# Kernel tuning notes

Hardware: AMD Instinct MI355X
Metric: run time of the kernel (lower is better)

Reference implementation:

```python
import jax, jax.numpy as jnp
import numpy as np


def setup_inputs() -> dict:
    key = jax.random.key(0)
    ks = jax.random.split(key, 5)
    B, S, H, F, E = 2, 2048, 768, 1536, 8
    scale_h = 1.0 / np.sqrt(H)
    scale_f = 1.0 / np.sqrt(F)
    return {
        "hidden_states": jax.random.normal(ks[0], (B, S, H), dtype=jnp.float32),
        "gate_w": jax.random.normal(ks[1], (E, H), dtype=jnp.float32) * scale_h,
        "w1": jax.random.normal(ks[2], (E, F, H), dtype=jnp.float32) * scale_h,
        "w3": jax.random.normal(ks[3], (E, F, H), dtype=jnp.float32) * scale_h,
        "w2": jax.random.normal(ks[4], (E, H, F), dtype=jnp.float32) * scale_f,
        "k": 2,
    }


def reference(hidden_states, gate_w, w1, w3, w2, k):
    B, S, H = hidden_states.shape
    E = gate_w.shape[0]
    x = hidden_states.reshape(-1, H)                     # [T, H]
    T = x.shape[0]

    # Router: softmax in fp32, top-k, renormalize among selected experts.
    router_logits = x @ gate_w.T                         # [T, E]
    probs = jax.nn.softmax(router_logits.astype(jnp.float32), axis=-1)
    top_w, top_i = jax.lax.top_k(probs, k)               # [T, k]
    top_w = top_w / jnp.sum(top_w, axis=-1, keepdims=True)
    top_w = top_w.astype(x.dtype)

    # Scatter top-k weights into dense [T, E] combine weights (0 for unselected).
    combine = jnp.zeros((T, E), dtype=x.dtype)
    combine = combine.at[jnp.arange(T)[:, None], top_i].set(top_w)

    # SwiGLU experts (zero-weight experts contribute exactly 0 to the sum).
    g = jnp.einsum("th,efh->tef", x, w1)                 # [T, E, F]
    u = jnp.einsum("th,efh->tef", x, w3)                 # [T, E, F]
    act = jax.nn.silu(g) * u                             # [T, E, F]
    expert_out = jnp.einsum("tef,ehf->teh", act, w2)     # [T, E, H]
    y = jnp.einsum("te,teh->th", combine, expert_out)    # [T, H]

    return y.reshape(B, S, H), router_logits
```

## Files before the change

### kernel.cpp

```cpp
#include <hip/hip_runtime.h>
#include <hip/hip_bf16.h>

#define T_TOK 4096
#define H_DIM 768
#define E_NUM 8
#define F_DIM 1536
#define WELEM (E_NUM * F_DIM * H_DIM)

typedef __bf16 bf16x8 __attribute__((ext_vector_type(8)));
typedef float f32x4 __attribute__((ext_vector_type(4)));
typedef unsigned int u32;

#define VMCNT(n) asm volatile("s_waitcnt vmcnt(" #n ")" ::: "memory")
#define CFENCE() asm volatile("" ::: "memory")

__device__ __forceinline__ unsigned short f2bf(float f) {
    unsigned int u = __float_as_uint(f);
    u += 0x7FFF + ((u >> 16) & 1);
    return (unsigned short)(u >> 16);
}

__device__ __forceinline__ void gload16(const unsigned short* g, unsigned short* l) {
    __builtin_amdgcn_global_load_lds(
        (const __attribute__((address_space(1))) u32*)(g),
        (__attribute__((address_space(3))) u32*)(l),
        16, 0, 0);
}

__global__ void convert3_kernel(const float* __restrict__ s0,
                                const float* __restrict__ s1,
                                const float* __restrict__ s2,
                                unsigned short* __restrict__ d0,
                                unsigned short* __restrict__ d1,
                                unsigned short* __restrict__ d2) {
    int i = (blockIdx.x * blockDim.x + threadIdx.x) * 4;
    int stride = gridDim.x * blockDim.x * 4;
    for (; i < 3 * WELEM; i += stride) {
        int r = i / WELEM;
        int j = i - r * WELEM;
        const float* s = (r == 0) ? s0 : (r == 1) ? s1 : s2;
        unsigned short* d = (r == 0) ? d0 : (r == 1) ? d1 : d2;
        float4 v = *reinterpret_cast<const float4*>(s + j);
        ushort4 o;
        o.x = f2bf(v.x); o.y = f2bf(v.y); o.z = f2bf(v.z); o.w = f2bf(v.w);
        *reinterpret_cast<ushort4*>(d + j) = o;
    }
}

__global__ __launch_bounds__(256) void router_kernel(
    const float* __restrict__ x,
    const float* __restrict__ gw,
    float* __restrict__ logits_out,
    float* __restrict__ weight,
    int* __restrict__ eidx,
    unsigned short* __restrict__ xb) {
    int t = blockIdx.x * 4 + (threadIdx.x >> 6);
    int lane = threadIdx.x & 63;

    const float4* xr = reinterpret_cast<const float4*>(x + (size_t)t * H_DIM);
    float4 xv[3];
#pragma unroll
    for (int i = 0; i < 3; ++i) xv[i] = xr[i * 64 + lane];

    unsigned short* xbr = xb + (size_t)t * H_DIM;
#pragma unroll
    for (int i = 0; i < 3; ++i) {
        ushort4 o;
        o.x = f2bf(xv[i].x); o.y = f2bf(xv[i].y);
        o.z = f2bf(xv[i].z); o.w = f2bf(xv[i].w);
        *reinterpret_cast<ushort4*>(xbr + (i * 64 + lane) * 4) = o;
    }

    float v[E_NUM];
#pragma unroll
    for (int e = 0; e < E_NUM; ++e) {
        const float4* g = reinterpret_cast<const float4*>(gw + e * H_DIM);
        float p = 0.f;
#pragma unroll
        for (int i = 0; i < 3; ++i) {
            float4 gv = g[i * 64 + lane];
            p += xv[i].x * gv.x + xv[i].y * gv.y + xv[i].z * gv.z + xv[i].w * gv.w;
        }
        v[e] = p;
    }
#pragma unroll
    for (int d = 1; d < 8; d <<= 1)
#pragma unroll
        for (int e = 0; e < E_NUM; ++e) v[e] += __shfl_xor(v[e], d);
    int me = lane & 7;
    float le = v[0];
#pragma unroll
    for (int e = 1; e < E_NUM; ++e) le = (me == e) ? v[e] : le;
#pragma unroll
    for (int d = 8; d < 64; d <<= 1) le += __shfl_xor(le, d);

    if (lane < 8) logits_out[t * E_NUM + lane] = le;

    float m0 = le;
#pragma unroll
    for (int d = 1; d < 8; d <<= 1) m0 = fmaxf(m0, __shfl_xor(m0, d));
    unsigned long long b0 = __ballot(le == m0);
    int e0 = (__ffsll((long long)b0) - 1) & 7;
    float le1 = (me == e0) ? -3.4e38f : le;
    float m1 = le1;
#pragma unroll
    for (int d = 1; d < 8; d <<= 1) m1 = fmaxf(m1, __shfl_xor(m1, d));
    unsigned long long b1 = __ballot(le1 == m1);
    int e1 = (__ffsll((long long)b1) - 1) & 7;

    if (lane == 0) {
        float w0 = 1.f / (1.f + __expf(m1 - m0));
        weight[t * 2 + 0] = w0;
        weight[t * 2 + 1] = 1.f - w0;
        eidx[t] = e0 | (e1 << 8);
    }
}

__global__ __launch_bounds__(256) void build_lists_kernel(
    const int* __restrict__ eidx,
    int* __restrict__ list,
    int* __restrict__ counts) {
    int e = blockIdx.x;
    int tid = threadIdx.x;
    int lane = tid & 63;
    int wv = tid >> 6;
    __shared__ int wsum[4];
    __shared__ int wbase[4];
    __shared__ int sbase;
    if (tid == 0) sbase = 0;
    __syncthreads();
    for (int c = 0; c < T_TOK; c += 256) {
        int tok = c + tid;
        int pk = eidx[tok];
        int slot = -1;
        if ((pk & 255) == e) slot = tok * 2;
        else if ((pk >> 8) == e) slot = tok * 2 + 1;
        unsigned long long m = __ballot(slot >= 0);
        int prefix = __popcll(m & ((1ull << lane) - 1ull));
        if (lane == 0) wsum[wv] = __popcll(m);
        __syncthreads();
        if (tid == 0) {
            int s = sbase;
#pragma unroll
            for (int i = 0; i < 4; ++i) { wbase[i] = s; s += wsum[i]; }
            sbase = s;
        }
        __syncthreads();
        if (slot >= 0) list[e * T_TOK + wbase[wv] + prefix] = slot;
        __syncthreads();
    }
    if (tid == 0) counts[e] = sbase;
}

__global__ __launch_bounds__(256, 3) void gemm13_kernel(
    const unsigned short* __restrict__ xb,
    const unsigned short* __restrict__ w1b,
    const unsigned short* __restrict__ w3b,
    const int* __restrict__ list,
    const int* __restrict__ counts,
    unsigned short* __restrict__ act) {
    int orig = blockIdx.x;
    int wg = (orig & 7) * 768 + (orig >> 3);
    int tm = wg & 31;
    int tn = (wg >> 5) % 24;
    int e = wg / (32 * 24);

    int cnt = counts[e];
    if (tm * 128 >= cnt) return;
    const int* lst = list + e * T_TOK + tm * 128;
    int mrem = cnt - tm * 128;

    __shared__ unsigned short sA[3][128 * 32];
    __shared__ unsigned short sB1[3][64 * 32];
    __shared__ unsigned short sB3[3][64 * 32];

    int tid = threadIdx.x;
    int lane = tid & 63;
    int wid = tid >> 6;

    int r0 = tid >> 2;
    int r1 = r0 + 64;
    int c8 = ((tid & 3) ^ ((r0 >> 1) & 3)) * 8;
    int tok0 = lst[(r0 < mrem) ? r0 : 0] >> 1;
    int tok1 = lst[(r1 < mrem) ? r1 : 0] >> 1;
    const unsigned short* gA0 = xb + (size_t)tok0 * H_DIM + c8;
    const unsigned short* gA1 = xb + (size_t)tok1 * H_DIM + c8;
    const unsigned short* gB1 = w1b + ((size_t)e * F_DIM + tn * 64 + r0) * H_DIM + c8;
    const unsigned short* gB3 = w3b + ((size_t)e * F_DIM + tn * 64 + r0) * H_DIM + c8;

    auto stage = [&](int b, int kt) {
        gload16(gA0 + kt, &sA[b][wid * 512]);
        gload16(gA1 + kt, &sA[b][2048 + wid * 512]);
        gload16(gB1 + kt, &sB1[b][wid * 512]);
        gload16(gB3 + kt, &sB3[b][wid * 512]);
    };

    int wr = (wid >> 1) * 64;
    int wc = (wid & 1) * 32;
    int fr = lane & 15;
    int kb = ((lane >> 4) ^ ((lane >> 1) & 3)) * 8;

    f32x4 accG[4][2] = {};
    f32x4 accU[4][2] = {};

    const int NT = H_DIM / 32;
    stage(0, 0);
    stage(1, 32);
    int cur = 0;
    for (int t = 0; t < NT; ++t) {
        if (t + 2 < NT) {
            int nb = cur + 2; if (nb >= 3) nb -= 3;
            stage(nb, (t + 2) * 32);
            VMCNT(8);
        } else if (t + 1 < NT) {
            VMCNT(4);
        } else {
            VMCNT(0);
        }
        __builtin_amdgcn_s_barrier();
        CFENCE();

        bf16x8 a[4], b1[2], b3[2];
#pragma unroll
        for (int mi = 0; mi < 4; ++mi)
            a[mi] = *reinterpret_cast<const bf16x8*>(&sA[cur][(wr + mi * 16 + fr) * 32 + kb]);
#pragma unroll
        for (int ni = 0; ni < 2; ++ni) {
            b1[ni] = *reinterpret_cast<const bf16x8*>(&sB1[cur][(wc + ni * 16 + fr) * 32 + kb]);
            b3[ni] = *reinterpret_cast<const bf16x8*>(&sB3[cur][(wc + ni * 16 + fr) * 32 + kb]);
        }
#pragma unroll
        for (int mi = 0; mi < 4; ++mi)
#pragma unroll
            for (int ni = 0; ni < 2; ++ni) {
                accG[mi][ni] = __builtin_amdgcn_mfma_f32_16x16x32_bf16(a[mi], b1[ni], accG[mi][ni], 0, 0, 0);
                accU[mi][ni] = __builtin_amdgcn_mfma_f32_16x16x32_bf16(a[mi], b3[ni], accU[mi][ni], 0, 0, 0);
            }
        CFENCE();
        __builtin_amdgcn_s_barrier();
        cur = (cur + 1 < 3) ? cur + 1 : 0;
    }

    int rg = (lane >> 4) * 4;
    int ci = lane & 15;
#pragma unroll
    for (int mi = 0; mi < 4; ++mi) {
#pragma unroll
        for (int r = 0; r < 4; ++r) {
            int m = wr + mi * 16 + rg + r;
            if (m >= mrem) continue;
            int entry = lst[m];
            size_t rowOff = (size_t)entry * F_DIM + tn * 64;
#pragma unroll
            for (int ni = 0; ni < 2; ++ni) {
                float g = accG[mi][ni][r];
                float u = accU[mi][ni][r];
                float s = g / (1.f + __expf(-g));
                act[rowOff + wc + ni * 16 + ci] = f2bf(s * u);
            }
        }
    }
}

__global__ __launch_bounds__(256, 3) void gemm2_kernel(
    const unsigned short* __restrict__ act,
    const unsigned short* __restrict__ w2b,
    const int* __restrict__ list,
    const int* __restrict__ counts,
    const float* __restrict__ weight,
    float* __restrict__ ybuf) {
    int orig = blockIdx.x;
    int wg = (orig & 7) * 192 + (orig >> 3);
    int tm = wg & 31;
    int tn = (wg >> 5) % 6;
    int e = wg / (32 * 6);

    int cnt = counts[e];
    if (tm * 128 >= cnt) return;
    const int* lst = list + e * T_TOK + tm * 128;
    int mrem = cnt - tm * 128;

    __shared__ unsigned short sA[3][128 * 32];
    __shared__ unsigned short sB[3][128 * 32];

    int tid = threadIdx.x;
    int lane = tid & 63;
    int wid = tid >> 6;

    int r0 = tid >> 2;
    int r1 = r0 + 64;
    int c8 = ((tid & 3) ^ ((r0 >> 1) & 3)) * 8;
    int row0 = lst[(r0 < mrem) ? r0 : 0];
    int row1 = lst[(r1 < mrem) ? r1 : 0];
    const unsigned short* gA0 = act + (size_t)row0 * F_DIM + c8;
    const unsigned short* gA1 = act + (size_t)row1 * F_DIM + c8;
    const unsigned short* gB0 = w2b + ((size_t)e * H_DIM + tn * 128 + r0) * F_DIM + c8;
    const unsigned short* gB1 = gB0 + (size_t)64 * F_DIM;

    auto stage = [&](int b, int kt) {
        gload16(gA0 + kt, &sA[b][wid * 512]);
        gload16(gA1 + kt, &sA[b][2048 + wid * 512]);
        gload16(gB0 + kt, &sB[b][wid * 512]);
        gload16(gB1 + kt, &sB[b][2048 + wid * 512]);
    };

    int wr = (wid >> 1) * 64;
    int wc = (wid & 1) * 64;
    int fr = lane & 15;
    int kb = ((lane >> 4) ^ ((lane >> 1) & 3)) * 8;

    f32x4 acc[4][4] = {};

    const int NT = F_DIM / 32;
    stage(0, 0);
    stage(1, 32);
    int cur = 0;
    for (int t = 0; t < NT; ++t) {
        if (t + 2 < NT) {
            int nb = cur + 2; if (nb >= 3) nb -= 3;
            stage(nb, (t + 2) * 32);
            VMCNT(8);
        } else if (t + 1 < NT) {
            VMCNT(4);
        } else {
            VMCNT(0);
        }
        __builtin_amdgcn_s_barrier();
        CFENCE();

        bf16x8 a[4], b[4];
#pragma unroll
        for (int mi = 0; mi < 4; ++mi)
            a[mi] = *reinterpret_cast<const bf16x8*>(&sA[cur][(wr + mi * 16 + fr) * 32 + kb]);
#pragma unroll
        for (int ni = 0; ni < 4; ++ni)
            b[ni] = *reinterpret_cast<const bf16x8*>(&sB[cur][(wc + ni * 16 + fr) * 32 + kb]);
#pragma unroll
        for (int mi = 0; mi < 4; ++mi)
#pragma unroll
            for (int ni = 0; ni < 4; ++ni)
                acc[mi][ni] = __builtin_amdgcn_mfma_f32_16x16x32_bf16(a[mi], b[ni], acc[mi][ni], 0, 0, 0);
        CFENCE();
        __builtin_amdgcn_s_barrier();
        cur = (cur + 1 < 3) ? cur + 1 : 0;
    }

    int rg = (lane >> 4) * 4;
    int ci = lane & 15;
#pragma unroll
    for (int mi = 0; mi < 4; ++mi) {
#pragma unroll
        for (int r = 0; r < 4; ++r) {
            int m = wr + mi * 16 + rg + r;
            if (m >= mrem) continue;
            int entry = lst[m];
            float wv = weight[entry];
            size_t rowOff = (size_t)entry * H_DIM + tn * 128;
#pragma unroll
            for (int ni = 0; ni < 4; ++ni)
                ybuf[rowOff + wc + ni * 16 + ci] = acc[mi][ni][r] * wv;
        }
    }
}

__global__ void combine_kernel(const float* __restrict__ ybuf, float* __restrict__ y) {
    int v = blockIdx.x * blockDim.x + threadIdx.x;
    if (v >= T_TOK * H_DIM / 4) return;
    int t = v / (H_DIM / 4);
    int hv = v % (H_DIM / 4);
    float4 a = reinterpret_cast<const float4*>(ybuf + (size_t)(2 * t) * H_DIM)[hv];
    float4 b = reinterpret_cast<const float4*>(ybuf + (size_t)(2 * t + 1) * H_DIM)[hv];
    float4 r;
    r.x = a.x + b.x; r.y = a.y + b.y; r.z = a.z + b.z; r.w = a.w + b.w;
    reinterpret_cast<float4*>(y)[v] = r;
}

extern "C" void kernel_launch(void* const* d_in, const int* in_sizes, int n_in,
                              void* d_out, int out_size, void* d_ws, size_t ws_size,
                              hipStream_t stream) {
    const float* x  = (const float*)d_in[0];
    const float* gw = (const float*)d_in[1];
    const float* w1 = (const float*)d_in[2];
    const float* w3 = (const float*)d_in[3];
    const float* w2 = (const float*)d_in[4];

    float* y = (float*)d_out;
    float* logits_out = y + (size_t)T_TOK * H_DIM;

    char* ws = (char*)d_ws;
    size_t off = 0;
    auto alloc = [&](size_t bytes) -> char* {
        char* p = ws + off;
        off += (bytes + 255) & ~(size_t)255;
        return p;
    };
    unsigned short* xb  = (unsigned short*)alloc((size_t)T_TOK * H_DIM * 2);
    unsigned short* w1b = (unsigned short*)alloc((size_t)WELEM * 2);
    unsigned short* w3b = (unsigned short*)alloc((size_t)WELEM * 2);
    unsigned short* w2b = (unsigned short*)alloc((size_t)WELEM * 2);
    unsigned short* act = (unsigned short*)alloc((size_t)T_TOK * 2 * F_DIM * 2);
    float* ybuf   = (float*)alloc((size_t)T_TOK * 2 * H_DIM * 4);
    float* weight = (float*)alloc((size_t)T_TOK * 2 * 4);
    int* list     = (int*)alloc((size_t)E_NUM * T_TOK * 4);
    int* counts   = (int*)alloc((size_t)E_NUM * 4);
    int* eidx     = (int*)alloc((size_t)T_TOK * 4);

    convert3_kernel<<<4096, 256, 0, stream>>>(w1, w3, w2, w1b, w3b, w2b);

    router_kernel<<<T_TOK / 4, 256, 0, stream>>>(x, gw, logits_out, weight, eidx, xb);

    build_lists_kernel<<<E_NUM, 256, 0, stream>>>(eidx, list, counts);

    gemm13_kernel<<<6144, 256, 0, stream>>>(xb, w1b, w3b, list, counts, act);

    gemm2_kernel<<<1536, 256, 0, stream>>>(act, w2b, list, counts, weight, ybuf);

    combine_kernel<<<(T_TOK * H_DIM / 4 + 255) / 256, 256, 0, stream>>>(ybuf, y);
}
```

Before: 155.2 us.

## Merge weight conversion into router kernel and scatter-add expert outputs atomically

Folds the bf16 weight-conversion kernel into the router kernel as extra blocks, so both run in a single launch and can overlap. Drops the per-slot ybuf and the separate combine kernel: gemm2 now atomically adds weighted results straight into a zeroed output, with a memset added before the prologue. This removes one launch and a full write-then-read pass over ybuf. In exchange it adds float atomics, which make the summation order nondeterministic and may cost throughput.

```diff
diff --git a/kernel.cpp b/kernel.cpp
--- a/kernel.cpp
+++ b/kernel.cpp
@@ -27,35 +27,38 @@
         16, 0, 0);
 }
 
-__global__ void convert3_kernel(const float* __restrict__ s0,
-                                const float* __restrict__ s1,
-                                const float* __restrict__ s2,
-                                unsigned short* __restrict__ d0,
-                                unsigned short* __restrict__ d1,
-                                unsigned short* __restrict__ d2) {
-    int i = (blockIdx.x * blockDim.x + threadIdx.x) * 4;
-    int stride = gridDim.x * blockDim.x * 4;
-    for (; i < 3 * WELEM; i += stride) {
-        int r = i / WELEM;
-        int j = i - r * WELEM;
-        const float* s = (r == 0) ? s0 : (r == 1) ? s1 : s2;
-        unsigned short* d = (r == 0) ? d0 : (r == 1) ? d1 : d2;
-        float4 v = *reinterpret_cast<const float4*>(s + j);
-        ushort4 o;
-        o.x = f2bf(v.x); o.y = f2bf(v.y); o.z = f2bf(v.z); o.w = f2bf(v.w);
-        *reinterpret_cast<ushort4*>(d + j) = o;
-    }
-}
-
-__global__ __launch_bounds__(256) void router_kernel(
+__global__ __launch_bounds__(256) void prologue_kernel(
     const float* __restrict__ x,
     const float* __restrict__ gw,
+    const float* __restrict__ w1,
+    const float* __restrict__ w3,
+    const float* __restrict__ w2,
     float* __restrict__ logits_out,
     float* __restrict__ weight,
     int* __restrict__ eidx,
-    unsigned short* __restrict__ xb) {
-    int t = blockIdx.x * 4 + (threadIdx.x >> 6);
-    int lane = threadIdx.x & 63;
+    unsigned short* __restrict__ xb,
+    unsigned short* __restrict__ w1b,
+    unsigned short* __restrict__ w3b,
+    unsigned short* __restrict__ w2b) {
+    int tid = threadIdx.x;
+    if (blockIdx.x >= 1024) {
+        int cb = blockIdx.x - 1024;
+        int i = (cb * 256 + tid) * 4;
+        int stride = (gridDim.x - 1024) * 256 * 4;
+        for (; i < 3 * WELEM; i += stride) {
+            int r = i / WELEM;
+            int j = i - r * WELEM;
+            const float* s = (r == 0) ? w1 : (r == 1) ? w3 : w2;
+            unsigned short* d = (r == 0) ? w1b : (r == 1) ? w3b : w2b;
+            float4 v = *reinterpret_cast<const float4*>(s + j);
+            ushort4 o;
+            o.x = f2bf(v.x); o.y = f2bf(v.y); o.z = f2bf(v.z); o.w = f2bf(v.w);
+            *reinterpret_cast<ushort4*>(d + j) = o;
+        }
+        return;
+    }
+    int t = blockIdx.x * 4 + (tid >> 6);
+    int lane = tid & 63;
 
     const float4* xr = reinterpret_cast<const float4*>(x + (size_t)t * H_DIM);
     float4 xv[3];
@@ -268,7 +271,7 @@
     const int* __restrict__ list,
     const int* __restrict__ counts,
     const float* __restrict__ weight,
-    float* __restrict__ ybuf) {
+    float* __restrict__ y) {
     int orig = blockIdx.x;
     int wg = (orig & 7) * 192 + (orig >> 3);
     int tm = wg & 31;
@@ -354,25 +357,14 @@
             int m = wr + mi * 16 + rg + r;
             if (m >= mrem) continue;
             int entry = lst[m];
+            int tok = entry >> 1;
             float wv = weight[entry];
-            size_t rowOff = (size_t)entry * H_DIM + tn * 128;
+            size_t rowOff = (size_t)tok * H_DIM + tn * 128;
 #pragma unroll
             for (int ni = 0; ni < 4; ++ni)
-                ybuf[rowOff + wc + ni * 16 + ci] = acc[mi][ni][r] * wv;
-        }
-    }
-}
-
-__global__ void combine_kernel(const float* __restrict__ ybuf, float* __restrict__ y) {
-    int v = blockIdx.x * blockDim.x + threadIdx.x;
-    if (v >= T_TOK * H_DIM / 4) return;
-    int t = v / (H_DIM / 4);
-    int hv = v % (H_DIM / 4);
-    float4 a = reinterpret_cast<const float4*>(ybuf + (size_t)(2 * t) * H_DIM)[hv];
-    float4 b = reinterpret_cast<const float4*>(ybuf + (size_t)(2 * t + 1) * H_DIM)[hv];
-    float4 r;
-    r.x = a.x + b.x; r.y = a.y + b.y; r.z = a.z + b.z; r.w = a.w + b.w;
-    reinterpret_cast<float4*>(y)[v] = r;
+                atomicAdd(&y[rowOff + wc + ni * 16 + ci], acc[mi][ni][r] * wv);
+        }
+    }
 }
 
 extern "C" void kernel_launch(void* const* d_in, const int* in_sizes, int n_in,
@@ -399,21 +391,20 @@
     unsigned short* w3b = (unsigned short*)alloc((size_t)WELEM * 2);
     unsigned short* w2b = (unsigned short*)alloc((size_t)WELEM * 2);
     unsigned short* act = (unsigned short*)alloc((size_t)T_TOK * 2 * F_DIM * 2);
-    float* ybuf   = (float*)alloc((size_t)T_TOK * 2 * H_DIM * 4);
     float* weight = (float*)alloc((size_t)T_TOK * 2 * 4);
     int* list     = (int*)alloc((size_t)E_NUM * T_TOK * 4);
     int* counts   = (int*)alloc((size_t)E_NUM * 4);
     int* eidx     = (int*)alloc((size_t)T_TOK * 4);
 
-    convert3_kernel<<<4096, 256, 0, stream>>>(w1, w3, w2, w1b, w3b, w2b);
-
-    router_kernel<<<T_TOK / 4, 256, 0, stream>>>(x, gw, logits_out, weight, eidx, xb);
+    hipMemsetAsync(y, 0, (size_t)T_TOK * H_DIM * 4, stream);
+
+    prologue_kernel<<<4480, 256, 0, stream>>>(x, gw, w1, w3, w2,
+                                              logits_out, weight, eidx, xb,
+                                              w1b, w3b, w2b);
 
     build_lists_kernel<<<E_NUM, 256, 0, stream>>>(eidx, list, counts);
 
     gemm13_kernel<<<6144, 256, 0, stream>>>(xb, w1b, w3b, list, counts, act);
 
-    gemm2_kernel<<<1536, 256, 0, stream>>>(act, w2b, list, counts, weight, ybuf);
-
-    combine_kernel<<<(T_TOK * H_DIM / 4 + 255) / 256, 256, 0, stream>>>(ybuf, y);
-}
+    gemm2_kernel<<<1536, 256, 0, stream>>>(act, w2b, list, counts, weight, y);
+}
```

After: 162.7 us. 4.9% more time.
